# Optimization experiments

Measured on AMD Instinct MI355X. Metric: run time of the kernel, lower is better.

Reference implementation:

```python
import jax, jax.numpy as jnp
import numpy as np

NUM_HEADS = 16
LN_EPS = 1e-5


def pos_encoding(length, d):
    pos = jnp.arange(length, dtype=jnp.float32)[:, None]
    i = jnp.arange(d, dtype=jnp.float32)[None, :]
    angle = pos / jnp.power(10000.0, (2.0 * jnp.floor(i / 2.0)) / d)
    return jnp.where((jnp.arange(d) % 2) == 0, jnp.sin(angle), jnp.cos(angle))


def rel_shift(x):
    # x: (B, H, l, m) -> TXL shift trick
    b, h, l, m = x.shape
    x = jnp.concatenate([x, jnp.zeros((b, h, l, 1), x.dtype)], axis=-1)
    x = x.reshape(b, h, l * (m + 1))
    return x[:, :, l - 1:-1].reshape(b, h, l, m)


def layer_norm(x, g, b):
    mu = jnp.mean(x, axis=-1, keepdims=True)
    var = jnp.mean(jnp.square(x - mu), axis=-1, keepdims=True)
    return (x - mu) * jax.lax.rsqrt(var + LN_EPS) * g + b


def setup_inputs() -> dict:
    key = jax.random.key(0)
    B, S, M, D, L, V = 2, 1024, 1024, 1024, 4, 32000
    ks = jax.random.split(key, 32)
    s = 0.02
    d = {
        'inputs': jax.random.randint(ks[0], (B, S), 0, V, dtype=jnp.int32),
        'mems': jax.random.normal(ks[1], (L, B, M, D), jnp.float32),
        'emb': jax.random.normal(ks[2], (V, D), jnp.float32) * s,
        'Wq': jax.random.normal(ks[3], (L, D, D), jnp.float32) * s,
        'bq': jnp.zeros((L, D), jnp.float32),
        'Wke': jax.random.normal(ks[4], (L, D, D), jnp.float32) * s,
        'bke': jnp.zeros((L, D), jnp.float32),
        'Wkr': jax.random.normal(ks[5], (L, D, D), jnp.float32) * s,
        'bkr': jnp.zeros((L, D), jnp.float32),
        'Wv': jax.random.normal(ks[6], (L, D, D), jnp.float32) * s,
        'bv': jnp.zeros((L, D), jnp.float32),
        'Wo': jax.random.normal(ks[7], (L, D, D), jnp.float32) * s,
        'bo': jnp.zeros((L, D), jnp.float32),
        'ln1_g': jnp.ones((L, D), jnp.float32),
        'ln1_b': jnp.zeros((L, D), jnp.float32),
        'W1': jax.random.normal(ks[8], (L, D, D), jnp.float32) * s,
        'b1': jnp.zeros((L, D), jnp.float32),
        'W2': jax.random.normal(ks[9], (L, D, D), jnp.float32) * s,
        'b2': jnp.zeros((L, D), jnp.float32),
        'ln2_g': jnp.ones((L, D), jnp.float32),
        'ln2_b': jnp.zeros((L, D), jnp.float32),
        'Wh': jax.random.normal(ks[10], (D, D), jnp.float32) * s,
        'bh': jnp.zeros((D,), jnp.float32),
        'Wf': jax.random.normal(ks[11], (D, V), jnp.float32) * s,
        'bf': jnp.zeros((V,), jnp.float32),
        'next_mem_len': 1024,
    }
    return d


def reference(inputs, mems, emb, Wq, bq, Wke, bke, Wkr, bkr, Wv, bv, Wo, bo,
              ln1_g, ln1_b, W1, b1, W2, b2, ln2_g, ln2_b, Wh, bh, Wf, bf,
              next_mem_len):
    B, S = inputs.shape
    L, _, M, D = mems.shape
    T = M + S
    H = NUM_HEADS
    dh = D // H
    sqrt_dk = jnp.sqrt(jnp.float32(dh))

    rel_enc = pos_encoding(T, D)[::-1]  # (T, D), reversed
    # look-ahead mask: query i may attend key j iff j <= i + M
    mask = (jnp.arange(T)[None, :] > (jnp.arange(S)[:, None] + M)).astype(jnp.float32)
    mask = mask[None, None] * -1e9  # (1,1,S,T)

    x = emb[inputs] * jnp.sqrt(jnp.float32(D))  # (B,S,D)

    for l in range(L):
        x_tilde = jnp.concatenate([mems[l], x], axis=1)  # (B,T,D)
        q = (x @ Wq[l] + bq[l]).reshape(B, S, H, dh).transpose(0, 2, 1, 3)
        k = (x_tilde @ Wke[l] + bke[l]).reshape(B, T, H, dh).transpose(0, 2, 1, 3)
        v = (x_tilde @ Wv[l] + bv[l]).reshape(B, T, H, dh).transpose(0, 2, 1, 3)
        A = jnp.einsum('bhsd,bhtd->bhst', q, k)
        Qr = (rel_enc @ Wkr[l] + bkr[l]).reshape(T, H, dh).transpose(1, 0, 2)  # (H,T,dh)
        B_hat = jnp.einsum('bhsd,htd->bhst', q, Qr)
        score = (A + rel_shift(B_hat)) / sqrt_dk + mask
        attn = jax.nn.softmax(score, axis=-1)
        ctx = jnp.einsum('bhst,bhtd->bhsd', attn, v)
        ctx = ctx.transpose(0, 2, 1, 3).reshape(B, S, D)
        attn_out = ctx @ Wo[l] + bo[l]
        h1 = layer_norm(x + attn_out, ln1_g[l], ln1_b[l])
        ff = jax.nn.gelu(h1 @ W1[l] + b1[l], approximate=False) @ W2[l] + b2[l]
        x = layer_norm(h1 + ff, ln2_g[l], ln2_b[l])

    x = jax.nn.gelu(x @ Wh + bh, approximate=False)
    logits = x @ Wf + bf
    return logits
```

## Files before the change

kernel.cpp:

```cpp
#include <hip/hip_runtime.h>
#include <hip/hip_bf16.h>
#include <math.h>

typedef __attribute__((ext_vector_type(4))) float f32x4;
typedef __attribute__((ext_vector_type(8))) short s16x8;

#define BB 2
#define SS 1024
#define MEM 1024
#define DD 1024
#define LL 4
#define VV 32000
#define TT 2048
#define NH 16
#define DH 64

__device__ __forceinline__ short f2bf(float f) {
    unsigned u = __float_as_uint(f);
    u += 0x7fffu + ((u >> 16) & 1u);
    return (short)(u >> 16);
}

__device__ __forceinline__ float gelu_f(float x) {
    return 0.5f * x * (1.0f + erff(x * 0.70710678118654752f));
}

__device__ __forceinline__ void gll16(const short* g, short* l) {
    __builtin_amdgcn_global_load_lds(
        (__attribute__((address_space(1))) void*)(short*)g,
        (__attribute__((address_space(3))) void*)l, 16, 0, 0);
}

template<int WM, int WN>
__global__ __launch_bounds__(256) void gemm_bf16(
    const short* __restrict__ A, const short* __restrict__ Bt,
    const float* __restrict__ bias, const float* __restrict__ bias2,
    int nsplit, void* __restrict__ Cv, int N, int K, int nby, int act, int obf)
{
    constexpr int BM = WM * 32, BN = WN * 32;
    constexpr int NA = BM / 32, NB = BN / 32;
    __shared__ short a_s[BM * 64];
    __shared__ short b_s[BN * 64];
    const int tid  = threadIdx.x;
    const int lane = tid & 63;
    const int wave = tid >> 6;
    const int wr = wave >> 1, wc = wave & 1;
    const int fr = lane & 15, fg = lane >> 4;

    const int nwg = gridDim.x;
    const int bid = blockIdx.x;
    const int swz = ((nwg & 7) == 0) ? ((bid & 7) * (nwg >> 3) + (bid >> 3)) : bid;
    const size_t m0 = (size_t)(swz % nby) * BM;
    const size_t n0 = (size_t)(swz / nby) * BN;

    const short* gA[NA]; short* lA[NA];
    const short* gB[NB]; short* lB[NB];
    #pragma unroll
    for (int i = 0; i < NA; ++i) {
        const int s   = i * 256 + tid;
        const int row = (s >> 7) * 16 + (s & 15);
        const int kof = ((s >> 4) & 7) * 8;
        gA[i] = A + (m0 + row) * (size_t)K + kof;
        lA[i] = &a_s[s * 8];
    }
    #pragma unroll
    for (int i = 0; i < NB; ++i) {
        const int s   = i * 256 + tid;
        const int nn  = (s >> 7) * 16 + (s & 15);
        const int kof = ((s >> 4) & 7) * 8;
        gB[i] = Bt + (n0 + nn) * (size_t)K + kof;
        lB[i] = &b_s[s * 8];
    }

    f32x4 acc[WM][WN] = {};

    #pragma unroll
    for (int i = 0; i < NA; ++i) gll16(gA[i], lA[i]);
    #pragma unroll
    for (int i = 0; i < NB; ++i) gll16(gB[i], lB[i]);

    const int nt = K >> 6;
    for (int t = 0; t < nt; ++t) {
        __syncthreads();
        s16x8 af[WM][2], bf[WN][2];
        #pragma unroll
        for (int mi = 0; mi < WM; ++mi)
            #pragma unroll
            for (int h = 0; h < 2; ++h)
                af[mi][h] = *(const s16x8*)&a_s[((wr*WM + mi)*128 + (h*4 + fg)*16 + fr) * 8];
        #pragma unroll
        for (int ni = 0; ni < WN; ++ni)
            #pragma unroll
            for (int h = 0; h < 2; ++h)
                bf[ni][h] = *(const s16x8*)&b_s[((wc*WN + ni)*128 + (h*4 + fg)*16 + fr) * 8];
        if (t + 1 < nt) {
            __syncthreads();
            const int koff = (t + 1) << 6;
            #pragma unroll
            for (int i = 0; i < NA; ++i) gll16(gA[i] + koff, lA[i]);
            #pragma unroll
            for (int i = 0; i < NB; ++i) gll16(gB[i] + koff, lB[i]);
        }
        #pragma unroll
        for (int mi = 0; mi < WM; ++mi)
            #pragma unroll
            for (int ni = 0; ni < WN; ++ni) {
                acc[mi][ni] = __builtin_amdgcn_mfma_f32_16x16x32_bf16(
                    af[mi][0], bf[ni][0], acc[mi][ni], 0, 0, 0);
                acc[mi][ni] = __builtin_amdgcn_mfma_f32_16x16x32_bf16(
                    af[mi][1], bf[ni][1], acc[mi][ni], 0, 0, 0);
            }
    }

    float* Cf = (float*)Cv;
    short* Cb = (short*)Cv;
    #pragma unroll
    for (int mi = 0; mi < WM; ++mi) {
        #pragma unroll
        for (int ni = 0; ni < WN; ++ni) {
            const size_t r0 = m0 + wr*WM*16 + mi*16 + fg*4;
            const size_t c  = n0 + wc*WN*16 + ni*16 + fr;
            const float bb = (c < (size_t)nsplit) ? bias[c] : bias2[c - nsplit];
            #pragma unroll
            for (int rg = 0; rg < 4; ++rg) {
                float vv = acc[mi][ni][rg] + bb;
                if (act) vv = gelu_f(vv);
                if (obf) Cb[(r0 + rg)*(size_t)N + c] = f2bf(vv);
                else     Cf[(r0 + rg)*(size_t)N + c] = vv;
            }
        }
    }
}

#define READ_A8(MH, BUF) \
  _Pragma("unroll") for (int mf = 0; mf < 4; ++mf) \
  _Pragma("unroll") for (int kh = 0; kh < 2; ++kh) \
    aA[mf][kh] = *(const s16x8*)&lds[(BUF)*16384 + WR*8192 + (((MH)*4+mf)*128 + (kh*4+fg)*16 + fr)*8];

#define READ_B8(BUF) \
  _Pragma("unroll") for (int nf = 0; nf < 4; ++nf) \
  _Pragma("unroll") for (int kh = 0; kh < 2; ++kh) \
    bB[nf][kh] = *(const s16x8*)&lds[32768 + (BUF)*16384 + BH*8192 + ((BC4+nf)*128 + (kh*4+fg)*16 + fr)*8];

#define QUAD8(MH, NH) \
  _Pragma("unroll") for (int mf = 0; mf < 4; ++mf) \
  _Pragma("unroll") for (int n2 = 0; n2 < 2; ++n2) { \
    acc[(MH)*4+mf][(NH)*2+n2] = __builtin_amdgcn_mfma_f32_16x16x32_bf16( \
        aA[mf][0], bB[(NH)*2+n2][0], acc[(MH)*4+mf][(NH)*2+n2], 0, 0, 0); \
    acc[(MH)*4+mf][(NH)*2+n2] = __builtin_amdgcn_mfma_f32_16x16x32_bf16( \
        aA[mf][1], bB[(NH)*2+n2][1], acc[(MH)*4+mf][(NH)*2+n2], 0, 0, 0); }

#define STAGE_A8(HH, BUF, KT) { \
    const short* g = pA0 + (HH)*(128*1024) + (KT)*64; \
    short* l = &lds[(BUF)*16384 + (HH)*8192 + tid*8]; \
    gll16(g, l); gll16(g + 64*1024, l + 512*8); }

#define STAGE_B8(HH, BUF, KT) { \
    const short* g = pB0 + (HH)*(128*1024) + (KT)*64; \
    short* l = &lds[32768 + (BUF)*16384 + (HH)*8192 + tid*8]; \
    gll16(g, l); gll16(g + 64*1024, l + 512*8); }

#define PHASE8(BUF, MH, NH, RA, RB, SMAT, SH, SBUF, SKT, VMW) { \
    if (RA) { READ_A8(MH, BUF) } \
    if (RB) { READ_B8(BUF) } \
    if ((SMAT) == 0) STAGE_A8(SH, SBUF, SKT) else STAGE_B8(SH, SBUF, SKT) \
    __builtin_amdgcn_s_barrier(); \
    asm volatile("s_waitcnt lgkmcnt(0)" ::: "memory"); \
    __builtin_amdgcn_sched_barrier(0); \
    __builtin_amdgcn_s_setprio(1); \
    QUAD8(MH, NH) \
    __builtin_amdgcn_s_setprio(0); \
    if (VMW) { asm volatile("s_waitcnt vmcnt(4)" ::: "memory"); } \
    __builtin_amdgcn_s_barrier(); }

__global__ __launch_bounds__(512, 2) void gemm8p(
    const short* __restrict__ A, const short* __restrict__ Bt,
    const float* __restrict__ bias, float* __restrict__ C, int N)
{
    extern __shared__ short lds[];
    const int tid  = threadIdx.x;
    const int lane = tid & 63;
    const int wave = tid >> 6;
    const int WR = wave >> 2;
    const int WC = wave & 3;
    const int BH = WC >> 1;
    const int BC4 = (WC & 1) * 4;
    const int fr = lane & 15, fg = lane >> 4;

    const int nwg = gridDim.x;
    const int bid = blockIdx.x;
    const int swz = ((nwg & 7) == 0) ? ((bid & 7) * (nwg >> 3) + (bid >> 3)) : bid;
    const size_t m0 = (size_t)(swz % 8) * 256;
    const size_t n0 = (size_t)(swz / 8) * 256;

    const int arow0 = (tid >> 7) * 16 + (tid & 15);
    const int aks0  = ((tid >> 4) & 7) * 8;
    const short* pA0 = A  + (m0 + arow0) * 1024 + aks0;
    const short* pB0 = Bt + (n0 + arow0) * 1024 + aks0;

    f32x4 acc[8][4] = {};
    s16x8 aA[4][2], bB[4][2];

    STAGE_B8(0, 0, 0) STAGE_B8(1, 0, 0)
    STAGE_A8(0, 0, 0) STAGE_A8(1, 0, 0)
    STAGE_B8(0, 1, 1) STAGE_B8(1, 1, 1)
    asm volatile("s_waitcnt vmcnt(4)" ::: "memory");
    __builtin_amdgcn_s_barrier();

    for (int it = 0; it < 8; ++it) {
        const int k1 = 2*it + 1;
        int k2 = 2*it + 2; if (k2 > 15) k2 = 15;
        int k3 = 2*it + 3; if (k3 > 15) k3 = 15;
        PHASE8(0, 0, 0, 1, 1, 0, 0, 1, k1, 0)
        PHASE8(0, 0, 1, 0, 0, 0, 1, 1, k1, 0)
        PHASE8(0, 1, 0, 1, 0, 1, 0, 0, k2, 0)
        PHASE8(0, 1, 1, 0, 0, 1, 1, 0, k2, 1)
        PHASE8(1, 0, 0, 1, 1, 0, 0, 0, k2, 0)
        PHASE8(1, 0, 1, 0, 0, 0, 1, 0, k2, 0)
        PHASE8(1, 1, 0, 1, 0, 1, 0, 1, k3, 0)
        PHASE8(1, 1, 1, 0, 0, 1, 1, 1, k3, 1)
    }

    #pragma unroll
    for (int mf = 0; mf < 8; ++mf) {
        #pragma unroll
        for (int nf = 0; nf < 4; ++nf) {
            const size_t r0 = m0 + WR*128 + mf*16 + fg*4;
            const size_t c  = n0 + WC*64 + nf*16 + fr;
            const float bb = bias[c];
            #pragma unroll
            for (int rg = 0; rg < 4; ++rg)
                C[(r0 + rg) * (size_t)N + c] = acc[mf][nf][rg] + bb;
        }
    }
}

__global__ __launch_bounds__(256) void transpose7_kernel(
    const float* w0, const float* w1, const float* w2, const float* w3,
    const float* w4, const float* w5, const float* w6, short* out)
{
    __shared__ float t[32][33];
    const int z = blockIdx.z;
    const float* W;
    switch (z) {
        case 0: W = w0; break; case 1: W = w1; break; case 2: W = w2; break;
        case 3: W = w3; break; case 4: W = w4; break; case 5: W = w5; break;
        default: W = w6; break;
    }
    short* O = out + (size_t)z * DD * DD;
    const int tid = threadIdx.x;
    const int k0 = blockIdx.y * 32, n0 = blockIdx.x * 32;
    const int r = tid >> 3, c4 = (tid & 7) * 4;
    float4 v = *(const float4*)&W[(size_t)(k0 + r) * DD + n0 + c4];
    t[r][c4+0] = v.x; t[r][c4+1] = v.y; t[r][c4+2] = v.z; t[r][c4+3] = v.w;
    __syncthreads();
    short4 o;
    o.x = f2bf(t[c4+0][r]); o.y = f2bf(t[c4+1][r]);
    o.z = f2bf(t[c4+2][r]); o.w = f2bf(t[c4+3][r]);
    *(short4*)&O[(size_t)(n0 + r) * DD + k0 + c4] = o;
}

__global__ __launch_bounds__(256) void transposeF_kernel(
    const float* __restrict__ W, short* __restrict__ O)
{
    __shared__ float t[32][33];
    const int tid = threadIdx.x;
    const int k0 = blockIdx.y * 32, n0 = blockIdx.x * 32;
    const int r = tid >> 3, c4 = (tid & 7) * 4;
    float4 v = *(const float4*)&W[(size_t)(k0 + r) * VV + n0 + c4];
    t[r][c4+0] = v.x; t[r][c4+1] = v.y; t[r][c4+2] = v.z; t[r][c4+3] = v.w;
    __syncthreads();
    short4 o;
    o.x = f2bf(t[c4+0][r]); o.y = f2bf(t[c4+1][r]);
    o.z = f2bf(t[c4+2][r]); o.w = f2bf(t[c4+3][r]);
    *(short4*)&O[(size_t)(n0 + r) * DD + k0 + c4] = o;
}

__global__ __launch_bounds__(256) void attn_kernel(
    const short* __restrict__ q, const short* __restrict__ k,
    const short* __restrict__ v, const short* __restrict__ Qr,
    short* __restrict__ ctx, int kstr, int qstr)
{
    __shared__ short k_s[64][72];
    __shared__ short vT_s[64][72];
    __shared__ short qr_s[128][72];
    __shared__ float a_t[64][67];
    __shared__ short p_s[64][72];

    const int tid  = threadIdx.x;
    const int id   = blockIdx.x;
    const int bh   = id & 31;
    const int qi   = ((id >> 5) + bh) & 15;
    const int q0   = qi * 64;
    const int b    = bh >> 4;
    const int h    = bh & 15;
    const int hoff = h * DH;

    const int lane = tid & 63;
    const int wave = tid >> 6;
    const int fr   = lane & 15;
    const int fg   = lane >> 4;
    const int tk = tid >> 2, ck = (tid & 3) * 16;
    const int rq = tid >> 1, dq = (tid & 1) * 32;
    const int sr  = tid >> 2;
    const int sc0 = (tid & 3) * 16;

    const short* qrow = q + ((size_t)(b * SS + q0 + 16 * wave + fr)) * DD + hoff;
    s16x8 aq0 = *(const s16x8*)(qrow + fg * 8);
    s16x8 aq1 = *(const s16x8*)(qrow + 32 + fg * 8);

    float m_r = -1e30f, l_r = 0.0f;

    const int t_end = q0 + 64 + MEM;
    const int u0b   = SS - 1 - q0 - 63;

    s16x8 kf0, kf1, vf0, vf1, rf0, rf1, rf2, rf3;
    auto loadT = [&](int t0) {
        const short* kp = k + ((size_t)(b * TT + t0 + tk)) * kstr + hoff + ck;
        const short* vp = v + ((size_t)(b * TT + t0 + tk)) * kstr + hoff + ck;
        kf0 = *(const s16x8*)kp;  kf1 = *(const s16x8*)(kp + 8);
        vf0 = *(const s16x8*)vp;  vf1 = *(const s16x8*)(vp + 8);
        int u = t0 + u0b + rq;
        u = u < 0 ? 0 : (u > TT - 1 ? TT - 1 : u);
        const short* rp = Qr + (size_t)u * qstr + hoff + dq;
        rf0 = *(const s16x8*)rp;        rf1 = *(const s16x8*)(rp + 8);
        rf2 = *(const s16x8*)(rp + 16); rf3 = *(const s16x8*)(rp + 24);
    };
    loadT(0);

    f32x4 opv[4] = {};
    const int nlo = 3 - wave, nhi = 7 - wave;

    for (int t0 = 0; t0 < t_end; t0 += 64) {
        asm volatile("" ::: "memory");
        __builtin_amdgcn_s_barrier();
        __builtin_amdgcn_sched_barrier(0);
        {
            *(s16x8*)&k_s[tk][ck]     = kf0;
            *(s16x8*)&k_s[tk][ck + 8] = kf1;
            #pragma unroll
            for (int i = 0; i < 8; ++i) {
                const int d0 = ck + i, d1 = ck + 8 + i;
                vT_s[d0][tk ^ (((d0 >> 3) & 3) << 3)] = vf0[i];
                vT_s[d1][tk ^ (((d1 >> 3) & 3) << 3)] = vf1[i];
            }
            *(s16x8*)&qr_s[rq][dq]      = rf0;
            *(s16x8*)&qr_s[rq][dq + 8]  = rf1;
            *(s16x8*)&qr_s[rq][dq + 16] = rf2;
            *(s16x8*)&qr_s[rq][dq + 24] = rf3;
        }
        if (t0 + 64 < t_end) loadT(t0 + 64);
        asm volatile("s_waitcnt lgkmcnt(0)" ::: "memory");
        __builtin_amdgcn_s_barrier();
        __builtin_amdgcn_sched_barrier(0);

        {
            #pragma unroll
            for (int n = 0; n < 4; ++n) {
                s16x8 b0 = *(const s16x8*)&k_s[16*n + fr][fg * 8];
                s16x8 b1 = *(const s16x8*)&k_s[16*n + fr][32 + fg * 8];
                f32x4 ca = {0, 0, 0, 0};
                ca = __builtin_amdgcn_mfma_f32_16x16x32_bf16(aq0, b0, ca, 0, 0, 0);
                ca = __builtin_amdgcn_mfma_f32_16x16x32_bf16(aq1, b1, ca, 0, 0, 0);
                #pragma unroll
                for (int rg = 0; rg < 4; ++rg)
                    a_t[16*wave + 4*fg + rg][16*n + fr] = ca[rg];
            }
        }
        {
            #pragma unroll
            for (int n = 0; n < 8; ++n) {
                if (n < nlo || n > nhi) continue;
                s16x8 c0 = *(const s16x8*)&qr_s[16*n + fr][fg * 8];
                s16x8 c1 = *(const s16x8*)&qr_s[16*n + fr][32 + fg * 8];
                f32x4 cb = {0, 0, 0, 0};
                cb = __builtin_amdgcn_mfma_f32_16x16x32_bf16(aq0, c0, cb, 0, 0, 0);
                cb = __builtin_amdgcn_mfma_f32_16x16x32_bf16(aq1, c1, cb, 0, 0, 0);
                #pragma unroll
                for (int rg = 0; rg < 4; ++rg) {
                    const int r  = 16*wave + 4*fg + rg;
                    const int tl = 16*n + fr - 63 + r;
                    if ((unsigned)tl < 64u) a_t[r][tl] += cb[rg];
                }
            }
        }

        {
            const int sg = q0 + sr;
            float e[16];
            float mx = -1e30f;
            #pragma unroll
            for (int j = 0; j < 16; ++j) {
                const int c = sc0 + j;
                float x = a_t[sr][c] * 0.125f;
                x = (t0 + c > sg + MEM) ? -1e30f : x;
                e[j] = x;
                mx = fmaxf(mx, x);
            }
            mx = fmaxf(mx, __shfl_xor(mx, 1, 64));
            mx = fmaxf(mx, __shfl_xor(mx, 2, 64));
            const float mn  = fmaxf(m_r, mx);
            const float scl = __expf(m_r - mn);
            float sum = 0.0f;
            s16x8 p0, p1;
            #pragma unroll
            for (int j = 0; j < 16; ++j) {
                float ev = __expf(e[j] - mn);
                sum += ev;
                if (j < 8) p0[j] = f2bf(ev); else p1[j - 8] = f2bf(ev);
            }
            sum += __shfl_xor(sum, 1, 64);
            sum += __shfl_xor(sum, 2, 64);
            l_r = l_r * scl + sum;
            m_r = mn;
            *(s16x8*)&p_s[sr][sc0]     = p0;
            *(s16x8*)&p_s[sr][sc0 + 8] = p1;

            f32x4 scv;
            #pragma unroll
            for (int rg = 0; rg < 4; ++rg) scv[rg] = __shfl(scl, 16*fg + 4*rg, 64);
            #pragma unroll
            for (int n = 0; n < 4; ++n)
                #pragma unroll
                for (int rg = 0; rg < 4; ++rg) opv[n][rg] *= scv[rg];
            s16x8 ap0 = *(const s16x8*)&p_s[16*wave + fr][fg * 8];
            s16x8 ap1 = *(const s16x8*)&p_s[16*wave + fr][32 + fg * 8];
            #pragma unroll
            for (int n = 0; n < 4; ++n) {
                const int d  = 16*n + fr;
                const int xw = (d >> 3) & 3;
                s16x8 bv0 = *(const s16x8*)&vT_s[d][(fg ^ xw) * 8];
                s16x8 bv1 = *(const s16x8*)&vT_s[d][32 + (fg ^ xw) * 8];
                opv[n] = __builtin_amdgcn_mfma_f32_16x16x32_bf16(ap0, bv0, opv[n], 0, 0, 0);
                opv[n] = __builtin_amdgcn_mfma_f32_16x16x32_bf16(ap1, bv1, opv[n], 0, 0, 0);
            }
        }
    }

    {
        f32x4 lv;
        #pragma unroll
        for (int rg = 0; rg < 4; ++rg) lv[rg] = __shfl(l_r, 16*fg + 4*rg, 64);
        #pragma unroll
        for (int rg = 0; rg < 4; ++rg) {
            const int r = 16*wave + 4*fg + rg;
            const float inv = 1.0f / lv[rg];
            short* op = ctx + ((size_t)(b * SS + q0 + r)) * DD + hoff;
            #pragma unroll
            for (int n = 0; n < 4; ++n)
                op[16*n + fr] = f2bf(opv[n][rg] * inv);
        }
    }
}

__global__ __launch_bounds__(256) void addln_kernel(
    const float* __restrict__ a, const float* __restrict__ b,
    const float* __restrict__ g, const float* __restrict__ be,
    float* __restrict__ out32, short* __restrict__ outbf)
{
    __shared__ float red[8];
    const int row = blockIdx.x;
    const int tid = threadIdx.x;
    const size_t base = (size_t)row * DD;
    const int c = tid * 4;
    float4 xa = *(const float4*)(a + base + c);
    float4 xb = *(const float4*)(b + base + c);
    float x0 = xa.x + xb.x, x1 = xa.y + xb.y, x2 = xa.z + xb.z, x3 = xa.w + xb.w;
    float s  = x0 + x1 + x2 + x3;
    float sq = x0 * x0 + x1 * x1 + x2 * x2 + x3 * x3;
    #pragma unroll
    for (int o = 32; o > 0; o >>= 1) {
        s  += __shfl_down(s, o, 64);
        sq += __shfl_down(sq, o, 64);
    }
    const int wv = tid >> 6;
    if ((tid & 63) == 0) { red[wv * 2] = s; red[wv * 2 + 1] = sq; }
    __syncthreads();
    float ts = red[0] + red[2] + red[4] + red[6];
    float tq = red[1] + red[3] + red[5] + red[7];
    float mu  = ts * (1.0f / DD);
    float var = tq * (1.0f / DD) - mu * mu;
    float rs  = rsqrtf(var + 1e-5f);
    float4 gv = *(const float4*)(g + c);
    float4 bv = *(const float4*)(be + c);
    float4 o4;
    o4.x = (x0 - mu) * rs * gv.x + bv.x;
    o4.y = (x1 - mu) * rs * gv.y + bv.y;
    o4.z = (x2 - mu) * rs * gv.z + bv.z;
    o4.w = (x3 - mu) * rs * gv.w + bv.w;
    *(float4*)(out32 + base + c) = o4;
    short4 ob;
    ob.x = f2bf(o4.x); ob.y = f2bf(o4.y); ob.z = f2bf(o4.z); ob.w = f2bf(o4.w);
    *(short4*)(outbf + base + c) = ob;
}

__global__ __launch_bounds__(256) void embed_kernel(
    const int* __restrict__ inp, const float* __restrict__ emb,
    float* __restrict__ x32, short* __restrict__ xbf)
{
    const int row = blockIdx.x;
    const int c = threadIdx.x * 4;
    const int idx = inp[row];
    float4 vv = *(const float4*)(emb + (size_t)idx * DD + c);
    vv.x *= 32.0f; vv.y *= 32.0f; vv.z *= 32.0f; vv.w *= 32.0f;
    *(float4*)(x32 + (size_t)row * DD + c) = vv;
    short4 ob;
    ob.x = f2bf(vv.x); ob.y = f2bf(vv.y); ob.z = f2bf(vv.z); ob.w = f2bf(vv.w);
    *(short4*)(xbf + (size_t)row * DD + c) = ob;
}

__global__ __launch_bounds__(256) void concat_kernel(
    const float* __restrict__ mems_l, const short* __restrict__ xbf,
    short* __restrict__ xt)
{
    size_t i = ((size_t)blockIdx.x * 256 + threadIdx.x) * 8;
    size_t bt = i / DD;
    int d = (int)(i - bt * DD);
    int b = (int)(bt / TT);
    int t = (int)(bt - (size_t)b * TT);
    s16x8 o;
    if (t < MEM) {
        const float* mp = mems_l + ((size_t)(b * MEM + t)) * DD + d;
        float4 a0 = *(const float4*)mp;
        float4 a1 = *(const float4*)(mp + 4);
        o[0] = f2bf(a0.x); o[1] = f2bf(a0.y); o[2] = f2bf(a0.z); o[3] = f2bf(a0.w);
        o[4] = f2bf(a1.x); o[5] = f2bf(a1.y); o[6] = f2bf(a1.z); o[7] = f2bf(a1.w);
    } else {
        o = *(const s16x8*)(xbf + ((size_t)(b * SS + (t - MEM))) * DD + d);
    }
    *(s16x8*)(xt + i) = o;
}

__global__ __launch_bounds__(256) void relenc_kernel(short* __restrict__ re)
{
    const int u = blockIdx.x;
    const int p = TT - 1 - u;
    const int i0 = threadIdx.x * 4;
    short4 o;
    #pragma unroll
    for (int j = 0; j < 4; ++j) {
        int i = i0 + j;
        float ex   = (float)(2 * (i >> 1)) * (1.0f / DD);
        float invf = __expf(-ex * 9.210340371976184f);
        float ang  = (float)p * invf;
        float val  = (i & 1) ? cosf(ang) : sinf(ang);
        ((short*)&o)[j] = f2bf(val);
    }
    *(short4*)&re[(size_t)u * DD + i0] = o;
}

extern "C" void kernel_launch(void* const* d_in, const int* in_sizes, int n_in,
                              void* d_out, int out_size, void* d_ws, size_t ws_size,
                              hipStream_t stream)
{
    const int*   inp  = (const int*)d_in[0];
    const float* mems = (const float*)d_in[1];
    const float* emb  = (const float*)d_in[2];
    const float* Wq   = (const float*)d_in[3];
    const float* bq   = (const float*)d_in[4];
    const float* Wke  = (const float*)d_in[5];
    const float* bke  = (const float*)d_in[6];
    const float* Wkr  = (const float*)d_in[7];
    const float* bkr  = (const float*)d_in[8];
    const float* Wv   = (const float*)d_in[9];
    const float* bv   = (const float*)d_in[10];
    const float* Wo   = (const float*)d_in[11];
    const float* bo   = (const float*)d_in[12];
    const float* ln1g = (const float*)d_in[13];
    const float* ln1b = (const float*)d_in[14];
    const float* W1   = (const float*)d_in[15];
    const float* b1   = (const float*)d_in[16];
    const float* W2   = (const float*)d_in[17];
    const float* b2   = (const float*)d_in[18];
    const float* ln2g = (const float*)d_in[19];
    const float* ln2b = (const float*)d_in[20];
    const float* Wh   = (const float*)d_in[21];
    const float* bh   = (const float*)d_in[22];
    const float* Wf   = (const float*)d_in[23];
    const float* bfb  = (const float*)d_in[24];

    hipFuncSetAttribute((const void*)gemm8p,
                        hipFuncAttributeMaxDynamicSharedMemorySize, 131072);

    char* wsb = (char*)d_ws;
    size_t off = 0;
    auto alloc = [&](size_t bytes) { char* p = wsb + off; off += (bytes + 255) & ~(size_t)255; return p; };
    float* h132  = (float*)alloc((size_t)BB*SS*DD*4);
    float* ao32  = (float*)alloc((size_t)BB*SS*DD*4);
    float* ff232 = (float*)alloc((size_t)BB*SS*DD*4);
    short* xt    = (short*)alloc((size_t)BB*TT*DD*2);
    short* qb    = (short*)alloc((size_t)BB*SS*DD*2);
    short* kvb   = (short*)alloc((size_t)BB*TT*DD*2*2);
    short* ctxb  = (short*)alloc((size_t)BB*SS*DD*2);
    short* ff1   = (short*)alloc((size_t)BB*SS*DD*2);
    float* x32   = (float*)alloc((size_t)BB*SS*DD*4);
    short* x_bf  = (short*)alloc((size_t)BB*SS*DD*2);
    short* whout = (short*)alloc((size_t)BB*SS*DD*2);
    short* rel   = (short*)alloc((size_t)TT*DD*2);
    short* qr4   = (short*)alloc((size_t)SS*2*4*DD*2);
    short* wt6   = (short*)alloc((size_t)6*DD*DD*2);
    short* wkr4  = (short*)h132;
    short* wft   = (short*)h132;

    relenc_kernel<<<TT, 256, 0, stream>>>(rel);
    embed_kernel<<<BB * SS, 256, 0, stream>>>(inp, emb, x32, x_bf);

    const size_t WOFF = (size_t)DD * DD;

    transpose7_kernel<<<dim3(32, 32, 4), 256, 0, stream>>>(
        Wkr + 0*WOFF, Wkr + 1*WOFF, Wkr + 2*WOFF, Wkr + 3*WOFF, Wq, Wq, Wq, wkr4);
    gemm_bf16<4,4><<<dim3(512), 256, 0, stream>>>(
        rel, wkr4, bkr, bkr, 4*DD, qr4, 4*DD, DD, TT/128, 0, 1);

    const int gSm = (DD / 64) * ((BB * SS) / 64);
    const int gKV = ((2 * DD) / 128) * ((BB * TT) / 128);

    for (int l = 0; l < LL; ++l) {
        const size_t wo  = (size_t)l * DD * DD;
        const size_t bo_ = (size_t)l * DD;
        transpose7_kernel<<<dim3(32, 32, 6), 256, 0, stream>>>(
            Wq + wo, Wke + wo, Wv + wo, Wo + wo, W1 + wo, W2 + wo, Wq, wt6);
        concat_kernel<<<(BB * TT * DD / 8) / 256, 256, 0, stream>>>(
            mems + (size_t)l * BB * MEM * DD, x_bf, xt);
        gemm_bf16<2,2><<<dim3(gSm), 256, 0, stream>>>(
            x_bf, wt6 + 0*WOFF, bq + bo_, bq + bo_, DD, qb, DD, DD, (BB*SS)/64, 0, 1);
        gemm_bf16<4,4><<<dim3(gKV), 256, 0, stream>>>(
            xt, wt6 + 1*WOFF, bke + bo_, bv + bo_, DD, kvb, 2*DD, DD, (BB*TT)/128, 0, 1);
        attn_kernel<<<dim3((SS / 64) * BB * NH), 256, 0, stream>>>(
            qb, kvb, kvb + DD, qr4 + (size_t)l * DD, ctxb, 2 * DD, 4 * DD);
        gemm_bf16<2,2><<<dim3(gSm), 256, 0, stream>>>(
            ctxb, wt6 + 3*WOFF, bo + bo_, bo + bo_, DD, ao32, DD, DD, (BB*SS)/64, 0, 0);
        addln_kernel<<<BB * SS, 256, 0, stream>>>(x32, ao32, ln1g + bo_, ln1b + bo_, h132, x_bf);
        gemm_bf16<2,2><<<dim3(gSm), 256, 0, stream>>>(
            x_bf, wt6 + 4*WOFF, b1 + bo_, b1 + bo_, DD, ff1, DD, DD, (BB*SS)/64, 1, 1);
        gemm_bf16<2,2><<<dim3(gSm), 256, 0, stream>>>(
            ff1, wt6 + 5*WOFF, b2 + bo_, b2 + bo_, DD, ff232, DD, DD, (BB*SS)/64, 0, 0);
        addln_kernel<<<BB * SS, 256, 0, stream>>>(h132, ff232, ln2g + bo_, ln2b + bo_, x32, x_bf);
    }

    transpose7_kernel<<<dim3(32, 32, 1), 256, 0, stream>>>(
        Wh, Wh, Wh, Wh, Wh, Wh, Wh, wt6);
    transposeF_kernel<<<dim3(VV / 32, DD / 32), 256, 0, stream>>>(Wf, wft);
    gemm_bf16<2,2><<<dim3(gSm), 256, 0, stream>>>(
        x_bf, wt6, bh, bh, DD, whout, DD, DD, (BB*SS)/64, 1, 1);
    gemm8p<<<dim3((VV / 256) * ((BB * SS) / 256)), 512, 131072, stream>>>(
        whout, wft, bfb, (float*)d_out, VV);
}
```

Baseline: 1.271 ms.

## Fuse Q/K/V projections into one large-tile GEMM and ring-buffer Qr in attention

Adds a new 256x128-tile GEMM kernel with 512 threads and a triple-buffered LDS pipeline. It computes Q, K and V in a single launch over the concatenated memory+input rows, and it also computes the relative-position projection. Because Q is now computed for the memory rows as well, this spends extra FLOPs to save a launch and gain larger tiles. The attention kernel reads Q from the fused buffer with the new stride, and it keeps Qr in a 128-row LDS ring so each step only loads 64 new Qr rows instead of reloading the whole window.

```diff
diff --git a/kernel.cpp b/kernel.cpp
--- a/kernel.cpp
+++ b/kernel.cpp
@@ -142,13 +142,13 @@
   _Pragma("unroll") for (int kh = 0; kh < 2; ++kh) \
     bB[nf][kh] = *(const s16x8*)&lds[32768 + (BUF)*16384 + BH*8192 + ((BC4+nf)*128 + (kh*4+fg)*16 + fr)*8];
 
-#define QUAD8(MH, NH) \
+#define QUAD8(MH, NHX) \
   _Pragma("unroll") for (int mf = 0; mf < 4; ++mf) \
   _Pragma("unroll") for (int n2 = 0; n2 < 2; ++n2) { \
-    acc[(MH)*4+mf][(NH)*2+n2] = __builtin_amdgcn_mfma_f32_16x16x32_bf16( \
-        aA[mf][0], bB[(NH)*2+n2][0], acc[(MH)*4+mf][(NH)*2+n2], 0, 0, 0); \
-    acc[(MH)*4+mf][(NH)*2+n2] = __builtin_amdgcn_mfma_f32_16x16x32_bf16( \
-        aA[mf][1], bB[(NH)*2+n2][1], acc[(MH)*4+mf][(NH)*2+n2], 0, 0, 0); }
+    acc[(MH)*4+mf][(NHX)*2+n2] = __builtin_amdgcn_mfma_f32_16x16x32_bf16( \
+        aA[mf][0], bB[(NHX)*2+n2][0], acc[(MH)*4+mf][(NHX)*2+n2], 0, 0, 0); \
+    acc[(MH)*4+mf][(NHX)*2+n2] = __builtin_amdgcn_mfma_f32_16x16x32_bf16( \
+        aA[mf][1], bB[(NHX)*2+n2][1], acc[(MH)*4+mf][(NHX)*2+n2], 0, 0, 0); }
 
 #define STAGE_A8(HH, BUF, KT) { \
     const short* g = pA0 + (HH)*(128*1024) + (KT)*64; \
@@ -160,7 +160,7 @@
     short* l = &lds[32768 + (BUF)*16384 + (HH)*8192 + tid*8]; \
     gll16(g, l); gll16(g + 64*1024, l + 512*8); }
 
-#define PHASE8(BUF, MH, NH, RA, RB, SMAT, SH, SBUF, SKT, VMW) { \
+#define PHASE8(BUF, MH, NHX, RA, RB, SMAT, SH, SBUF, SKT, VMW) { \
     if (RA) { READ_A8(MH, BUF) } \
     if (RB) { READ_B8(BUF) } \
     if ((SMAT) == 0) STAGE_A8(SH, SBUF, SKT) else STAGE_B8(SH, SBUF, SKT) \
@@ -168,7 +168,7 @@
     asm volatile("s_waitcnt lgkmcnt(0)" ::: "memory"); \
     __builtin_amdgcn_sched_barrier(0); \
     __builtin_amdgcn_s_setprio(1); \
-    QUAD8(MH, NH) \
+    QUAD8(MH, NHX) \
     __builtin_amdgcn_s_setprio(0); \
     if (VMW) { asm volatile("s_waitcnt vmcnt(4)" ::: "memory"); } \
     __builtin_amdgcn_s_barrier(); }
@@ -235,6 +235,113 @@
     }
 }
 
+__global__ __launch_bounds__(512, 2) void gemm8n(
+    const short* __restrict__ A, const short* __restrict__ Bt,
+    const float* __restrict__ bA, const float* __restrict__ bBp,
+    const float* __restrict__ bCp, int s1, int s2,
+    short* __restrict__ Cb, int N, int K, int nby)
+{
+    extern __shared__ short lds[];
+    const int tid  = threadIdx.x;
+    const int lane = tid & 63;
+    const int wave = tid >> 6;
+    const int WR = wave >> 2;
+    const int WC = wave & 3;
+    const int fr = lane & 15, fg = lane >> 4;
+
+    const int nwg = gridDim.x;
+    const int bid = blockIdx.x;
+    const int swz = ((nwg & 7) == 0) ? ((bid & 7) * (nwg >> 3) + (bid >> 3)) : bid;
+    const size_t m0 = (size_t)(swz % nby) * 256;
+    const size_t n0 = (size_t)(swz / nby) * 128;
+
+    const int rA  = (tid >> 7) * 16 + (tid & 15);
+    const int ks8 = ((tid >> 4) & 7) * 8;
+    const short* pA = A  + (m0 + rA) * (size_t)K + ks8;
+    const short* pB = Bt + (n0 + rA) * (size_t)K + ks8;
+
+    auto stageA = [&](int kt, int h, int buf) {
+        const short* g = pA + (size_t)(h * 128) * K + kt * 64;
+        short* l = &lds[buf * 16384 + h * 8192 + tid * 8];
+        gll16(g, l);
+        gll16(g + (size_t)64 * K, l + 512 * 8);
+    };
+    auto stageB = [&](int kt, int buf) {
+        const short* g = pB + kt * 64;
+        short* l = &lds[49152 + buf * 8192 + tid * 8];
+        gll16(g, l);
+        gll16(g + (size_t)64 * K, l + 512 * 8);
+    };
+
+    f32x4 acc[8][2] = {};
+    const int nt = K >> 6;
+
+    stageB(0, 0); stageA(0, 0, 0); stageA(0, 1, 0);
+    stageA(1, 0, 1); stageA(1, 1, 1); stageB(1, 1);
+
+    for (int J = 0; J < nt / 2; ++J) {
+        const int t0 = 2 * J, t1 = 2 * J + 1;
+        const int b0 = t0 % 3, b1 = t1 % 3;
+        const int b2 = (t0 + 2) % 3, b3 = (t1 + 2) % 3;
+        int s2k = t0 + 2; if (s2k >= nt) s2k = nt - 1;
+        int s3k = t1 + 2; if (s3k >= nt) s3k = nt - 1;
+
+        #pragma unroll
+        for (int ph = 0; ph < 2; ++ph) {
+            const int bt = ph ? b1 : b0;
+            asm volatile("s_waitcnt vmcnt(6)" ::: "memory");
+            __builtin_amdgcn_s_barrier();
+            __builtin_amdgcn_sched_barrier(0);
+            if (ph == 0) { stageB(s2k, b2); stageA(s2k, 0, b2); stageA(s2k, 1, b2); }
+            else         { stageA(s3k, 0, b3); stageA(s3k, 1, b3); stageB(s3k, b3); }
+            s16x8 bB[2][2];
+            #pragma unroll
+            for (int nf = 0; nf < 2; ++nf)
+                #pragma unroll
+                for (int kh = 0; kh < 2; ++kh)
+                    bB[nf][kh] = *(const s16x8*)&lds[49152 + bt*8192 +
+                        ((WC*2 + nf)*128 + (kh*4 + fg)*16 + fr) * 8];
+            #pragma unroll
+            for (int MH = 0; MH < 2; ++MH) {
+                s16x8 aF[4][2];
+                #pragma unroll
+                for (int mf = 0; mf < 4; ++mf)
+                    #pragma unroll
+                    for (int kh = 0; kh < 2; ++kh)
+                        aF[mf][kh] = *(const s16x8*)&lds[bt*16384 + WR*8192 +
+                            ((MH*4 + mf)*128 + (kh*4 + fg)*16 + fr) * 8];
+                asm volatile("s_waitcnt lgkmcnt(0)" ::: "memory");
+                __builtin_amdgcn_sched_barrier(0);
+                __builtin_amdgcn_s_setprio(1);
+                #pragma unroll
+                for (int mf = 0; mf < 4; ++mf)
+                    #pragma unroll
+                    for (int nf = 0; nf < 2; ++nf) {
+                        acc[MH*4+mf][nf] = __builtin_amdgcn_mfma_f32_16x16x32_bf16(
+                            aF[mf][0], bB[nf][0], acc[MH*4+mf][nf], 0, 0, 0);
+                        acc[MH*4+mf][nf] = __builtin_amdgcn_mfma_f32_16x16x32_bf16(
+                            aF[mf][1], bB[nf][1], acc[MH*4+mf][nf], 0, 0, 0);
+                    }
+                __builtin_amdgcn_s_setprio(0);
+            }
+        }
+    }
+
+    #pragma unroll
+    for (int mf = 0; mf < 8; ++mf) {
+        #pragma unroll
+        for (int nf = 0; nf < 2; ++nf) {
+            const size_t r0 = m0 + WR*128 + mf*16 + fg*4;
+            const size_t c  = n0 + WC*32 + nf*16 + fr;
+            const float bb = (c < (size_t)s1) ? bA[c]
+                            : (c < (size_t)s2) ? bBp[c - s1] : bCp[c - s2];
+            #pragma unroll
+            for (int rg = 0; rg < 4; ++rg)
+                Cb[(r0 + rg) * (size_t)N + c] = f2bf(acc[mf][nf][rg] + bb);
+        }
+    }
+}
+
 __global__ __launch_bounds__(256) void transpose7_kernel(
     const float* w0, const float* w1, const float* w2, const float* w3,
     const float* w4, const float* w5, const float* w6, short* out)
@@ -302,10 +409,11 @@
     const int fg   = lane >> 4;
     const int tk = tid >> 2, ck = (tid & 3) * 16;
     const int rq = tid >> 1, dq = (tid & 1) * 32;
+    const int jq = tid >> 2, dq3 = (tid & 3) * 16;
     const int sr  = tid >> 2;
     const int sc0 = (tid & 3) * 16;
 
-    const short* qrow = q + ((size_t)(b * SS + q0 + 16 * wave + fr)) * DD + hoff;
+    const short* qrow = q + ((size_t)(b * TT + q0 + 16 * wave + fr)) * kstr + hoff;
     s16x8 aq0 = *(const s16x8*)(qrow + fg * 8);
     s16x8 aq1 = *(const s16x8*)(qrow + 32 + fg * 8);
 
@@ -314,19 +422,28 @@
     const int t_end = q0 + 64 + MEM;
     const int u0b   = SS - 1 - q0 - 63;
 
-    s16x8 kf0, kf1, vf0, vf1, rf0, rf1, rf2, rf3;
-    auto loadT = [&](int t0) {
+    s16x8 kf0, kf1, vf0, vf1, rf0, rf1, rf2, rf3, rg0, rg1;
+    auto loadKV = [&](int t0) {
         const short* kp = k + ((size_t)(b * TT + t0 + tk)) * kstr + hoff + ck;
         const short* vp = v + ((size_t)(b * TT + t0 + tk)) * kstr + hoff + ck;
         kf0 = *(const s16x8*)kp;  kf1 = *(const s16x8*)(kp + 8);
         vf0 = *(const s16x8*)vp;  vf1 = *(const s16x8*)(vp + 8);
-        int u = t0 + u0b + rq;
+    };
+    {
+        int u = u0b + rq;
         u = u < 0 ? 0 : (u > TT - 1 ? TT - 1 : u);
         const short* rp = Qr + (size_t)u * qstr + hoff + dq;
         rf0 = *(const s16x8*)rp;        rf1 = *(const s16x8*)(rp + 8);
         rf2 = *(const s16x8*)(rp + 16); rf3 = *(const s16x8*)(rp + 24);
+    }
+    auto loadQRring = [&](int tn) {
+        int u = tn + u0b + 64 + jq;
+        u = u < 0 ? 0 : (u > TT - 1 ? TT - 1 : u);
+        const short* rp = Qr + (size_t)u * qstr + hoff + dq3;
+        rg0 = *(const s16x8*)rp;
+        rg1 = *(const s16x8*)(rp + 8);
     };
-    loadT(0);
+    loadKV(0);
 
     f32x4 opv[4] = {};
     const int nlo = 3 - wave, nhi = 7 - wave;
@@ -344,12 +461,18 @@
                 vT_s[d0][tk ^ (((d0 >> 3) & 3) << 3)] = vf0[i];
                 vT_s[d1][tk ^ (((d1 >> 3) & 3) << 3)] = vf1[i];
             }
-            *(s16x8*)&qr_s[rq][dq]      = rf0;
-            *(s16x8*)&qr_s[rq][dq + 8]  = rf1;
-            *(s16x8*)&qr_s[rq][dq + 16] = rf2;
-            *(s16x8*)&qr_s[rq][dq + 24] = rf3;
-        }
-        if (t0 + 64 < t_end) loadT(t0 + 64);
+            if (t0 == 0) {
+                *(s16x8*)&qr_s[rq][dq]      = rf0;
+                *(s16x8*)&qr_s[rq][dq + 8]  = rf1;
+                *(s16x8*)&qr_s[rq][dq + 16] = rf2;
+                *(s16x8*)&qr_s[rq][dq + 24] = rf3;
+            } else {
+                const int slot = (t0 + 64 + jq) & 127;
+                *(s16x8*)&qr_s[slot][dq3]     = rg0;
+                *(s16x8*)&qr_s[slot][dq3 + 8] = rg1;
+            }
+        }
+        if (t0 + 64 < t_end) { loadKV(t0 + 64); loadQRring(t0 + 64); }
         asm volatile("s_waitcnt lgkmcnt(0)" ::: "memory");
         __builtin_amdgcn_s_barrier();
         __builtin_amdgcn_sched_barrier(0);
@@ -371,8 +494,9 @@
             #pragma unroll
             for (int n = 0; n < 8; ++n) {
                 if (n < nlo || n > nhi) continue;
-                s16x8 c0 = *(const s16x8*)&qr_s[16*n + fr][fg * 8];
-                s16x8 c1 = *(const s16x8*)&qr_s[16*n + fr][32 + fg * 8];
+                const int pr = (t0 + 16*n + fr) & 127;
+                s16x8 c0 = *(const s16x8*)&qr_s[pr][fg * 8];
+                s16x8 c1 = *(const s16x8*)&qr_s[pr][32 + fg * 8];
                 f32x4 cb = {0, 0, 0, 0};
                 cb = __builtin_amdgcn_mfma_f32_16x16x32_bf16(aq0, c0, cb, 0, 0, 0);
                 cb = __builtin_amdgcn_mfma_f32_16x16x32_bf16(aq1, c1, cb, 0, 0, 0);
@@ -581,6 +705,8 @@
 
     hipFuncSetAttribute((const void*)gemm8p,
                         hipFuncAttributeMaxDynamicSharedMemorySize, 131072);
+    hipFuncSetAttribute((const void*)gemm8n,
+                        hipFuncAttributeMaxDynamicSharedMemorySize, 147456);
 
     char* wsb = (char*)d_ws;
     size_t off = 0;
@@ -589,15 +715,14 @@
     float* ao32  = (float*)alloc((size_t)BB*SS*DD*4);
     float* ff232 = (float*)alloc((size_t)BB*SS*DD*4);
     short* xt    = (short*)alloc((size_t)BB*TT*DD*2);
-    short* qb    = (short*)alloc((size_t)BB*SS*DD*2);
-    short* kvb   = (short*)alloc((size_t)BB*TT*DD*2*2);
+    short* qkvb  = (short*)alloc((size_t)BB*TT*3*DD*2);
     short* ctxb  = (short*)alloc((size_t)BB*SS*DD*2);
     short* ff1   = (short*)alloc((size_t)BB*SS*DD*2);
     float* x32   = (float*)alloc((size_t)BB*SS*DD*4);
     short* x_bf  = (short*)alloc((size_t)BB*SS*DD*2);
     short* whout = (short*)alloc((size_t)BB*SS*DD*2);
     short* rel   = (short*)alloc((size_t)TT*DD*2);
-    short* qr4   = (short*)alloc((size_t)SS*2*4*DD*2);
+    short* qr4   = (short*)alloc((size_t)TT*4*DD*2);
     short* wt6   = (short*)alloc((size_t)6*DD*DD*2);
     short* wkr4  = (short*)h132;
     short* wft   = (short*)h132;
@@ -609,11 +734,10 @@
 
     transpose7_kernel<<<dim3(32, 32, 4), 256, 0, stream>>>(
         Wkr + 0*WOFF, Wkr + 1*WOFF, Wkr + 2*WOFF, Wkr + 3*WOFF, Wq, Wq, Wq, wkr4);
-    gemm_bf16<4,4><<<dim3(512), 256, 0, stream>>>(
-        rel, wkr4, bkr, bkr, 4*DD, qr4, 4*DD, DD, TT/128, 0, 1);
+    gemm8n<<<dim3((TT/256) * (4*DD/128)), 512, 147456, stream>>>(
+        rel, wkr4, bkr, bkr, bkr, 4*DD, 4*DD, qr4, 4*DD, DD, TT/256);
 
     const int gSm = (DD / 64) * ((BB * SS) / 64);
-    const int gKV = ((2 * DD) / 128) * ((BB * TT) / 128);
 
     for (int l = 0; l < LL; ++l) {
         const size_t wo  = (size_t)l * DD * DD;
@@ -622,12 +746,11 @@
             Wq + wo, Wke + wo, Wv + wo, Wo + wo, W1 + wo, W2 + wo, Wq, wt6);
         concat_kernel<<<(BB * TT * DD / 8) / 256, 256, 0, stream>>>(
             mems + (size_t)l * BB * MEM * DD, x_bf, xt);
-        gemm_bf16<2,2><<<dim3(gSm), 256, 0, stream>>>(
-            x_bf, wt6 + 0*WOFF, bq + bo_, bq + bo_, DD, qb, DD, DD, (BB*SS)/64, 0, 1);
-        gemm_bf16<4,4><<<dim3(gKV), 256, 0, stream>>>(
-            xt, wt6 + 1*WOFF, bke + bo_, bv + bo_, DD, kvb, 2*DD, DD, (BB*TT)/128, 0, 1);
+        gemm8n<<<dim3((BB*TT/256) * (3*DD/128)), 512, 147456, stream>>>(
+            xt, wt6, bq + bo_, bke + bo_, bv + bo_, DD, 2*DD, qkvb, 3*DD, DD, BB*TT/256);
         attn_kernel<<<dim3((SS / 64) * BB * NH), 256, 0, stream>>>(
-            qb, kvb, kvb + DD, qr4 + (size_t)l * DD, ctxb, 2 * DD, 4 * DD);
+            qkvb + (size_t)MEM * 3 * DD, qkvb + DD, qkvb + 2 * DD,
+            qr4 + (size_t)l * DD, ctxb, 3 * DD, 4 * DD);
         gemm_bf16<2,2><<<dim3(gSm), 256, 0, stream>>>(
             ctxb, wt6 + 3*WOFF, bo + bo_, bo + bo_, DD, ao32, DD, DD, (BB*SS)/64, 0, 0);
         addln_kernel<<<BB * SS, 256, 0, stream>>>(x32, ao32, ln1g + bo_, ln1b + bo_, h132, x_bf);
```

Measured after the change: 1.267 ms. Within noise of the previous version (-0.3%).
